# Optimization experiments

Measured on AMD Instinct MI355X. Metric: run time of the kernel, lower is better.

Reference implementation:

```python
import jax, jax.numpy as jnp
import numpy as np

N = 16384      # tokens
D_IN = 256     # input feature dim
D = 1024       # d_model
H = 2048       # expert hidden dim (2 * d_model)
E = 8          # n_experts
K = 2          # top_k
OUT = 2        # output classes
EPS = 1e-5


def layernorm(x, g, b):
    m = jnp.mean(x, axis=-1, keepdims=True)
    v = jnp.mean(jnp.square(x - m), axis=-1, keepdims=True)
    return (x - m) * jax.lax.rsqrt(v + EPS) * g + b


def setup_inputs() -> dict:
    key = jax.random.key(0)
    ks = jax.random.split(key, 10)
    s_in = 1.0 / np.sqrt(D_IN)
    s_d = 1.0 / np.sqrt(D)
    s_h = 1.0 / np.sqrt(H)
    return {
        "x": jax.random.normal(ks[0], (N, D_IN), jnp.float32),
        "w_in": jax.random.normal(ks[1], (D_IN, D), jnp.float32) * s_in,
        "b_in": jnp.zeros((D,), jnp.float32),
        "g_in": jnp.ones((D,), jnp.float32),
        "beta_in": jnp.zeros((D,), jnp.float32),
        "w_gate": jax.random.normal(ks[2], (D, E), jnp.float32) * s_d,
        "w1": jax.random.normal(ks[3], (E, D, H), jnp.float32) * s_d,
        "b1": jnp.zeros((E, H), jnp.float32),
        "w2": jax.random.normal(ks[4], (E, H, D), jnp.float32) * s_h,
        "b2": jnp.zeros((E, D), jnp.float32),
        "g_moe": jnp.ones((D,), jnp.float32),
        "beta_moe": jnp.zeros((D,), jnp.float32),
        "g_out": jnp.ones((D,), jnp.float32),
        "beta_out": jnp.zeros((D,), jnp.float32),
        "w_cls": jax.random.normal(ks[5], (D, OUT), jnp.float32) * s_d,
        "b_cls": jnp.zeros((OUT,), jnp.float32),
    }


def reference(x, w_in, b_in, g_in, beta_in, w_gate, w1, b1, w2, b2,
              g_moe, beta_moe, g_out, beta_out, w_cls, b_cls):
    # input projection + norm
    h = layernorm(x @ w_in + b_in, g_in, beta_in)            # [N, D]
    # router: softmax then top-k, renormalize over selected experts
    probs = jax.nn.softmax(h @ w_gate, axis=-1)              # [N, E]
    _, top_idx = jax.lax.top_k(probs, K)                     # [N, K]
    sel = jax.nn.one_hot(top_idx, E, dtype=probs.dtype).sum(axis=1)  # [N, E] 0/1
    gates = probs * sel
    gates = gates / (jnp.sum(gates, axis=-1, keepdims=True) + 1e-9)
    # experts: weighted combine; gate==0 tokens contribute nothing (same math
    # as the torch masked gather/scatter-add, dropout off in eval)
    mixed = jnp.zeros_like(h)
    for e in range(E):  # fixed, small expert count
        expert_out = jax.nn.gelu(h @ w1[e] + b1[e]) @ w2[e] + b2[e]  # [N, D]
        mixed = mixed + gates[:, e:e + 1] * expert_out
    out = layernorm(h + mixed, g_moe, beta_moe)
    out = layernorm(out, g_out, beta_out)
    return out @ w_cls + b_cls                               # [N, OUT]
```

## Files before the change

kernel.cpp:

```cpp
#include <hip/hip_runtime.h>
#include <hip/hip_bf16.h>

#define D_IN 256
#define DM   1024
#define HD   2048
#define NE   8
#define NTOK 16384

typedef __attribute__((ext_vector_type(8))) short short8;
typedef __attribute__((ext_vector_type(4))) float f32x4;
typedef unsigned int uint;

#define MT_TOFF1 0
#define MT_TOFF2 512
#define MT_CNT1  1536
#define MT_P1    1600
#define MT_OFF1  1664
#define MT_CNT2  1728
#define MT_PCNT2 1856
#define MT_TOTAL 1984

__device__ inline ushort f2bf(float v){
  __hip_bfloat16 b = __float2bfloat16(v);
  return *reinterpret_cast<ushort*>(&b);
}
__device__ inline float bf2f(ushort u){
  __hip_bfloat16 b = *reinterpret_cast<__hip_bfloat16*>(&u);
  return __bfloat162float(b);
}

__device__ inline float gelu_fast(float x){
  float u = 0.7978845608028654f * x * (1.0f + 0.044715f*x*x);
  return x / (1.0f + __expf(-2.0f*u));
}

__device__ inline void gload16(const void* g, void* l){
  __builtin_amdgcn_global_load_lds(
      (const __attribute__((address_space(1))) void*)g,
      (__attribute__((address_space(3))) void*)l, 16, 0, 0);
}

__global__ __launch_bounds__(256) void transpose_bf16_kernel(
    const float* __restrict__ src, ushort* __restrict__ dst, int R, int C)
{
  __shared__ float tile[32][33];
  int e = blockIdx.z;
  src += (size_t)e*R*C; dst += (size_t)e*R*C;
  int c0 = blockIdx.x*32, r0 = blockIdx.y*32;
  int tx = threadIdx.x & 31, ty = threadIdx.x >> 5;
  #pragma unroll
  for (int rr = ty; rr < 32; rr += 8)
    tile[rr][tx] = src[(size_t)(r0+rr)*C + c0+tx];
  __syncthreads();
  #pragma unroll
  for (int rr = ty; rr < 32; rr += 8)
    dst[(size_t)(c0+rr)*R + r0+tx] = f2bf(tile[tx][rr]);
}

__global__ __launch_bounds__(256) void split_x_kernel(
    const float* __restrict__ x, ushort* __restrict__ xs3)
{
  int g = blockIdx.x*256 + threadIdx.x;
  int e0 = g*4;
  int row = e0 >> 8, col = e0 & 255;
  f32x4 v = *(const f32x4*)(x + (size_t)row*D_IN + col);
  ushort4 hi, mi, lo;
  #pragma unroll
  for (int i=0;i<4;++i){
    float f = v[i];
    ushort h = f2bf(f);       float fh = bf2f(h);
    ushort m = f2bf(f - fh);  float fm = bf2f(m);
    ushort l = f2bf(f - fh - fm);
    ((ushort*)&hi)[i]=h; ((ushort*)&mi)[i]=m; ((ushort*)&lo)[i]=l;
  }
  ushort* base = xs3 + (size_t)row*768 + col;
  *(ushort4*)(base)       = hi;
  *(ushort4*)(base + 256) = mi;
  *(ushort4*)(base + 512) = lo;
}

__global__ __launch_bounds__(256) void transpose_split3_kernel(
    const float* __restrict__ src, ushort* __restrict__ dst)
{
  __shared__ float tile[32][33];
  int c0 = blockIdx.x*32, r0 = blockIdx.y*32;
  int tx = threadIdx.x & 31, ty = threadIdx.x >> 5;
  #pragma unroll
  for (int rr = ty; rr < 32; rr += 8)
    tile[rr][tx] = src[(size_t)(r0+rr)*DM + c0+tx];
  __syncthreads();
  #pragma unroll
  for (int rr = ty; rr < 32; rr += 8){
    float f = tile[tx][rr];
    ushort h = f2bf(f);       float fh = bf2f(h);
    ushort m = f2bf(f - fh);  float fm = bf2f(m);
    ushort l = f2bf(f - fh - fm);
    ushort* d = dst + (size_t)(c0+rr)*768 + r0 + tx;
    d[0]   = h;
    d[256] = m;
    d[512] = l;
  }
}

__global__ __launch_bounds__(256) void wgate_t_kernel(
    const float* __restrict__ w_gate, float* __restrict__ wgt)
{
  int e = blockIdx.x;
  for (int j = threadIdx.x; j < DM; j += 256)
    wgt[(size_t)e*DM + j] = w_gate[(size_t)j*NE + e];
}

__global__ __launch_bounds__(256) void gemm_router(
    const ushort* __restrict__ A,
    const ushort* __restrict__ BT,
    const float* __restrict__ b_in,
    float* __restrict__ y)
{
  __shared__ ushort As[128*32];
  __shared__ ushort Bs[128*32];
  const int tid = threadIdx.x;
  const int w = tid>>6, l = tid&63;
  const int wm = w>>1, wn = w&1;
  const int bm0 = blockIdx.y*128, bn0 = blockIdx.x*128;
  const int lr = l&15, lk = l>>4;
  const int rsub = l>>2, csub = (l&3)*8;

  const ushort* ag[2]; const ushort* bg[2];
  ushort* al[2]; ushort* bl[2];
  #pragma unroll
  for (int i=0;i<2;++i){
    int ra = bm0 + w*32 + i*16 + rsub;
    int rb = bn0 + w*32 + i*16 + rsub;
    ag[i] = A  + (size_t)ra*768 + csub;
    bg[i] = BT + (size_t)rb*768 + csub;
    al[i] = (ushort*)As + (w*32 + i*16)*32;
    bl[i] = (ushort*)Bs + (w*32 + i*16)*32;
  }

  f32x4 zero = {0.f,0.f,0.f,0.f};
  f32x4 acc[4][4];
  #pragma unroll
  for (int i=0;i<4;++i){
    #pragma unroll
    for (int j=0;j<4;++j) acc[i][j]=zero;
  }

  const int pq[6][2] = {{0,0},{256,0},{0,256},{256,256},{512,0},{0,512}};
  for (int t=0;t<6;++t){
    int pOff = pq[t][0], qOff = pq[t][1];
    for (int kt=0; kt<256; kt+=32){
      #pragma unroll
      for (int i=0;i<2;++i){
        gload16(ag[i]+pOff+kt, al[i]);
        gload16(bg[i]+qOff+kt, bl[i]);
      }
      __syncthreads();
      short8 af[4], bf[4];
      #pragma unroll
      for (int i=0;i<4;++i) af[i] = *(const short8*)(As + (wm*64 + i*16 + lr)*32 + lk*8);
      #pragma unroll
      for (int j=0;j<4;++j) bf[j] = *(const short8*)(Bs + (wn*64 + j*16 + lr)*32 + lk*8);
      #pragma unroll
      for (int i=0;i<4;++i){
        #pragma unroll
        for (int j=0;j<4;++j)
          acc[i][j] = __builtin_amdgcn_mfma_f32_16x16x32_bf16(af[i], bf[j], acc[i][j], 0, 0, 0);
      }
      __syncthreads();
    }
  }

  #pragma unroll
  for (int i=0;i<4;++i){
    #pragma unroll
    for (int j=0;j<4;++j){
      int n = bn0 + wn*64 + j*16 + lr;
      float bn_ = b_in[n];
      #pragma unroll
      for (int r=0;r<4;++r){
        int m = bm0 + wm*64 + i*16 + lk*4 + r;
        y[(size_t)m*DM + n] = acc[i][j][r] + bn_;
      }
    }
  }
}

__device__ inline double wredd(double v){
  #pragma unroll
  for (int o=32;o>0;o>>=1) v += __shfl_xor(v, o, 64);
  return v;
}

__global__ __launch_bounds__(256) void ln_router_kernel(
    const float* __restrict__ g_in, const float* __restrict__ beta_in,
    const float* __restrict__ wgt,
    ushort* __restrict__ hbf, float* __restrict__ resid,
    float* __restrict__ gates, int* __restrict__ selmask)
{
  int tok = blockIdx.x*4 + (threadIdx.x>>6);
  int l = threadIdx.x & 63;
  float* row = resid + (size_t)tok*DM;
  float u[16];
  double s=0.0, q=0.0;
  #pragma unroll
  for (int r=0;r<16;++r){ u[r]=row[l+64*r]; s+=u[r]; q+=(double)u[r]*u[r]; }
  s = wredd(s); q = wredd(q);
  double mean = s*(1.0/1024.0);
  double var  = q*(1.0/1024.0) - mean*mean;
  double rstd = 1.0/sqrt(var + 1e-5);

  double lg[NE];
  #pragma unroll
  for (int e=0;e<NE;++e) lg[e]=0.0;
  float hv[16];
  #pragma unroll
  for (int r=0;r<16;++r){
    int j = l + 64*r;
    double v = ((double)u[r]-mean)*rstd*(double)g_in[j] + (double)beta_in[j];
    hv[r] = (float)v;
    #pragma unroll
    for (int e=0;e<NE;++e) lg[e] += v*(double)wgt[(size_t)e*DM + j];
  }
  #pragma unroll
  for (int r=0;r<16;++r){
    int j = l + 64*r;
    row[j] = hv[r];
    hbf[(size_t)tok*DM + j] = f2bf(hv[r]);
  }
  #pragma unroll
  for (int e=0;e<NE;++e) lg[e] = wredd(lg[e]);

  if (l==0){
    double mx = lg[0];
    #pragma unroll
    for (int e=1;e<NE;++e) mx = lg[e]>mx ? lg[e] : mx;
    double p[NE]; double sum=0.0;
    #pragma unroll
    for (int e=0;e<NE;++e){ p[e]=exp(lg[e]-mx); sum+=p[e]; }
    #pragma unroll
    for (int e=0;e<NE;++e) p[e]/=sum;
    int i1=0;
    for (int e=1;e<NE;++e) if (p[e]>p[i1]) i1=e;
    int i2=-1;
    for (int e=0;e<NE;++e){ if (e==i1) continue; if (i2<0 || p[e]>p[i2]) i2=e; }
    double denom = p[i1]+p[i2]+1e-9;
    float g[NE];
    #pragma unroll
    for (int e=0;e<NE;++e) g[e]=0.f;
    g[i1]=(float)(p[i1]/denom);
    g[i2]=(float)(p[i2]/denom);
    #pragma unroll
    for (int e=0;e<NE;++e) gates[(size_t)tok*NE+e]=g[e];
    selmask[tok] = (1<<i1)|(1<<i2);
  }
}

__global__ __launch_bounds__(256) void builder_count(
    const int* __restrict__ selmask, uint* __restrict__ bc1, uint* __restrict__ bc2)
{
  __shared__ uint c1[8], c2s[16];
  int b = blockIdx.x, tid = threadIdx.x;
  if (tid<8) c1[tid]=0;
  if (tid<16) c2s[tid]=0;
  __syncthreads();
  int m = selmask[b*256+tid];
  int ea = __ffs(m)-1, eb = 31-__clz(m);
  atomicAdd(&c1[ea],1u); atomicAdd(&c1[eb],1u);
  atomicAdd(&c2s[ea],1u); atomicAdd(&c2s[8+eb],1u);
  __syncthreads();
  if (tid<8) bc1[b*8+tid]=c1[tid];
  if (tid<16) bc2[b*16+tid]=c2s[tid];
}

__global__ __launch_bounds__(256) void builder_scan(
    const uint* __restrict__ bc1, const uint* __restrict__ bc2,
    uint* __restrict__ meta, int nch, int TPC)
{
  int tid = threadIdx.x;
  int c = tid/24, k = tid%24;
  if (c < nch){
    if (k < 8){
      uint run=0;
      for (int b=c*TPC; b<(c+1)*TPC; ++b){ meta[MT_TOFF1 + b*8 + k] = run; run += bc1[b*8+k]; }
      meta[MT_CNT1 + c*8 + k] = run;
    } else {
      int k2 = k-8;
      uint run=0;
      for (int b=c*TPC; b<(c+1)*TPC; ++b){ meta[MT_TOFF2 + b*16 + k2] = run; run += bc2[b*16+k2]; }
      meta[MT_CNT2 + c*16 + k2] = run;
      meta[MT_PCNT2 + c*16 + k2] = ((run + 127u)/128u)*128u;
    }
  }
  __syncthreads();
  if (tid < nch){
    uint off=0;
    for (int e=0;e<8;++e){
      uint cn = meta[MT_CNT1 + tid*8 + e];
      uint p = ((cn+127u)/128u)*128u;
      meta[MT_P1 + tid*8 + e] = p;
      meta[MT_OFF1 + tid*8 + e] = off;
      off += p;
    }
  }
}

__device__ inline int exclscan256(int v, int* sc, int tid){
  sc[tid]=v; __syncthreads();
  #pragma unroll
  for (int o=1;o<256;o<<=1){
    int x = (tid>=o) ? sc[tid-o] : 0;
    __syncthreads();
    sc[tid]+=x;
    __syncthreads();
  }
  int incl = sc[tid]; __syncthreads();
  return incl - v;
}

__global__ __launch_bounds__(256) void builder_fill(
    const int* __restrict__ selmask, const uint* __restrict__ meta,
    int* __restrict__ ids1, int CH)
{
  __shared__ int sc[256];
  int b = blockIdx.x, tid = threadIdx.x;
  int t = b*256 + tid;
  int c = t / CH;
  int m = selmask[t];
  int ea = __ffs(m)-1, eb = 31-__clz(m);
  int ja=0, jb=0;
  for (int e=0;e<8;++e){
    int r0 = exclscan256((ea==e)?1:0, sc, tid);
    if (ea==e) ja = r0;
    int r1 = exclscan256((eb==e)?1:0, sc, tid);
    if (eb==e) jb = r1;
  }
  {
    uint j    = meta[MT_TOFF2 + b*16 + ea] + (uint)ja;
    ids1[(c*8+ea)*CH + j] = t;
  }
  {
    uint j    = meta[MT_TOFF2 + b*16 + 8 + eb] + (uint)jb;
    uint pos1 = meta[MT_CNT2 + c*16 + eb] + j;
    ids1[(c*8+eb)*CH + pos1] = t;
  }
}

__global__ __launch_bounds__(256) void gemm_ffn1(
    const ushort* __restrict__ Abase,
    const ushort* __restrict__ BT,
    const int*   __restrict__ rows,
    const uint*  __restrict__ pcnt,
    const uint*  __restrict__ off1,
    const float* __restrict__ bias,
    ushort* __restrict__ t1,
    int K, int N, int CH)
{
  const int e = blockIdx.z;
  const int bm0 = blockIdx.y*128;
  if ((uint)bm0 >= pcnt[e]) return;
  const int bn0 = blockIdx.x*128;

  __shared__ ushort As[128*32];
  __shared__ ushort Bs[128*32];
  const int tid = threadIdx.x;
  const int w = tid>>6, l = tid&63;
  const int wm = w>>1, wn = w&1;
  const int lr = l&15, lk = l>>4;
  const int rsub = l>>2, csub = (l&3)*8;

  const ushort* ag[2]; const ushort* bg[2];
  ushort* al[2]; ushort* bl[2];
  #pragma unroll
  for (int i=0;i<2;++i){
    int ra = w*32 + i*16 + rsub;
    int id = rows[e*CH + bm0 + ra];
    ag[i] = Abase + (size_t)id*K + csub;
    int rb = bn0 + w*32 + i*16 + rsub;
    bg[i] = BT + (size_t)e*N*K + (size_t)rb*K + csub;
    al[i] = (ushort*)As + (w*32 + i*16)*32;
    bl[i] = (ushort*)Bs + (w*32 + i*16)*32;
  }

  f32x4 zero = {0.f,0.f,0.f,0.f};
  f32x4 acc[4][4];
  #pragma unroll
  for (int i=0;i<4;++i){
    #pragma unroll
    for (int j=0;j<4;++j) acc[i][j]=zero;
  }

  for (int kt = 0; kt < K; kt += 32) {
    #pragma unroll
    for (int i=0;i<2;++i){
      gload16(ag[i]+kt, al[i]);
      gload16(bg[i]+kt, bl[i]);
    }
    __syncthreads();
    short8 af[4], bf[4];
    #pragma unroll
    for (int i=0;i<4;++i) af[i] = *(const short8*)(As + (wm*64 + i*16 + lr)*32 + lk*8);
    #pragma unroll
    for (int j=0;j<4;++j) bf[j] = *(const short8*)(Bs + (wn*64 + j*16 + lr)*32 + lk*8);
    #pragma unroll
    for (int i=0;i<4;++i){
      #pragma unroll
      for (int j=0;j<4;++j)
        acc[i][j] = __builtin_amdgcn_mfma_f32_16x16x32_bf16(af[i], bf[j], acc[i][j], 0, 0, 0);
    }
    __syncthreads();
  }

  #pragma unroll
  for (int i=0;i<4;++i){
    #pragma unroll
    for (int j=0;j<4;++j){
      int n = bn0 + wn*64 + j*16 + lr;
      float bn_ = bias[(size_t)e*N + n];
      #pragma unroll
      for (int r=0;r<4;++r){
        int mloc = wm*64 + i*16 + lk*4 + r;
        float v = acc[i][j][r] + bn_;
        size_t trow = (size_t)off1[e] + bm0 + mloc;
        t1[trow*N + n] = f2bf(gelu_fast(v));
      }
    }
  }
}

template<int SLOT>
__global__ __launch_bounds__(256) void gemm_ffn2(
    const ushort* __restrict__ t1,
    const ushort* __restrict__ BT,
    const int*   __restrict__ ids1,
    const uint*  __restrict__ cnt2,
    const uint*  __restrict__ pcnt2,
    const uint*  __restrict__ off1,
    const float* __restrict__ bias,
    const float* __restrict__ gates,
    float* __restrict__ resid,
    int K, int N, int CH)
{
  const int e = blockIdx.z;
  const int bm0 = blockIdx.y*128;
  if ((uint)bm0 >= pcnt2[SLOT*8 + e]) return;
  const uint scnt  = cnt2[SLOT*8 + e];
  const uint start = (SLOT==1) ? cnt2[e] : 0u;
  const int bn0 = blockIdx.x*128;

  __shared__ ushort As[128*32];
  __shared__ ushort Bs[128*32];
  const int tid = threadIdx.x;
  const int w = tid>>6, l = tid&63;
  const int wm = w>>1, wn = w&1;
  const int lr = l&15, lk = l>>4;
  const int rsub = l>>2, csub = (l&3)*8;

  const ushort* ag[2]; const ushort* bg[2];
  ushort* al[2]; ushort* bl[2];
  #pragma unroll
  for (int i=0;i<2;++i){
    int ra = w*32 + i*16 + rsub;
    size_t arow = (size_t)off1[e] + start + bm0 + ra;
    ag[i] = t1 + arow*K + csub;
    int rb = bn0 + w*32 + i*16 + rsub;
    bg[i] = BT + (size_t)e*N*K + (size_t)rb*K + csub;
    al[i] = (ushort*)As + (w*32 + i*16)*32;
    bl[i] = (ushort*)Bs + (w*32 + i*16)*32;
  }

  f32x4 zero = {0.f,0.f,0.f,0.f};
  f32x4 acc[4][4];
  #pragma unroll
  for (int i=0;i<4;++i){
    #pragma unroll
    for (int j=0;j<4;++j) acc[i][j]=zero;
  }

  for (int kt = 0; kt < K; kt += 32) {
    #pragma unroll
    for (int i=0;i<2;++i){
      gload16(ag[i]+kt, al[i]);
      gload16(bg[i]+kt, bl[i]);
    }
    __syncthreads();
    short8 af[4], bf[4];
    #pragma unroll
    for (int i=0;i<4;++i) af[i] = *(const short8*)(As + (wm*64 + i*16 + lr)*32 + lk*8);
    #pragma unroll
    for (int j=0;j<4;++j) bf[j] = *(const short8*)(Bs + (wn*64 + j*16 + lr)*32 + lk*8);
    #pragma unroll
    for (int i=0;i<4;++i){
      #pragma unroll
      for (int j=0;j<4;++j)
        acc[i][j] = __builtin_amdgcn_mfma_f32_16x16x32_bf16(af[i], bf[j], acc[i][j], 0, 0, 0);
    }
    __syncthreads();
  }

  #pragma unroll
  for (int i=0;i<4;++i){
    #pragma unroll
    for (int j=0;j<4;++j){
      int n = bn0 + wn*64 + j*16 + lr;
      float bn_ = bias[(size_t)e*N + n];
      #pragma unroll
      for (int r=0;r<4;++r){
        int mloc = wm*64 + i*16 + lk*4 + r;
        int mg = bm0 + mloc;
        if ((uint)mg < scnt){
          int tok = ids1[e*CH + (int)start + mg];
          float g = gates[(size_t)tok*NE + e];
          resid[(size_t)tok*N + n] += g*(acc[i][j][r] + bn_);
        }
      }
    }
  }
}

__global__ __launch_bounds__(256) void final_kernel(
    const float* __restrict__ resid,
    const float* __restrict__ g_moe, const float* __restrict__ beta_moe,
    const float* __restrict__ g_out, const float* __restrict__ beta_out,
    const float* __restrict__ w_cls, const float* __restrict__ b_cls,
    float* __restrict__ out)
{
  int tok = blockIdx.x*4 + (threadIdx.x>>6);
  int l = threadIdx.x & 63;
  const float* row = resid + (size_t)tok*DM;
  float u[16];
  double s=0.0,q=0.0;
  #pragma unroll
  for (int r=0;r<16;++r){ u[r]=row[l + 64*r]; s+=u[r]; q+=(double)u[r]*u[r]; }
  s=wredd(s); q=wredd(q);
  double m1 = s*(1.0/1024.0), v1 = q*(1.0/1024.0)-m1*m1;
  double rs1 = 1.0/sqrt(v1+1e-5);
  float tv[16]; double s2=0.0,q2=0.0;
  #pragma unroll
  for (int r=0;r<16;++r){
    int j = l+64*r;
    float vv = (float)((u[r]-m1)*rs1)*g_moe[j] + beta_moe[j];
    tv[r]=vv; s2+=vv; q2+=(double)vv*vv;
  }
  s2=wredd(s2); q2=wredd(q2);
  double m2=s2*(1.0/1024.0), v2=q2*(1.0/1024.0)-m2*m2;
  double rs2=1.0/sqrt(v2+1e-5);
  double p0=0.0,p1=0.0;
  #pragma unroll
  for (int r=0;r<16;++r){
    int j=l+64*r;
    double y=((double)tv[r]-m2)*rs2*(double)g_out[j]+(double)beta_out[j];
    p0+=y*(double)w_cls[j*2]; p1+=y*(double)w_cls[j*2+1];
  }
  p0=wredd(p0); p1=wredd(p1);
  if (l==0){
    out[(size_t)tok*2  ]=(float)(p0+(double)b_cls[0]);
    out[(size_t)tok*2+1]=(float)(p1+(double)b_cls[1]);
  }
}

extern "C" void kernel_launch(void* const* d_in, const int* in_sizes, int n_in,
                              void* d_out, int out_size, void* d_ws, size_t ws_size,
                              hipStream_t stream)
{
  (void)in_sizes; (void)n_in; (void)out_size;
  const float* x       = (const float*)d_in[0];
  const float* w_in    = (const float*)d_in[1];
  const float* b_in    = (const float*)d_in[2];
  const float* g_in    = (const float*)d_in[3];
  const float* beta_in = (const float*)d_in[4];
  const float* w_gate  = (const float*)d_in[5];
  const float* w1      = (const float*)d_in[6];
  const float* b1      = (const float*)d_in[7];
  const float* w2      = (const float*)d_in[8];
  const float* b2      = (const float*)d_in[9];
  const float* g_moe   = (const float*)d_in[10];
  const float* beta_mo = (const float*)d_in[11];
  const float* g_out   = (const float*)d_in[12];
  const float* beta_ou = (const float*)d_in[13];
  const float* w_cls   = (const float*)d_in[14];
  const float* b_cls   = (const float*)d_in[15];
  float* out = (float*)d_out;

  char* p = (char*)d_ws;
  ushort* w1t   = (ushort*)p; p += (size_t)NE*HD*DM*2;
  ushort* w2t   = (ushort*)p; p += (size_t)NE*DM*HD*2;
  ushort* hbf   = (ushort*)p; p += (size_t)NTOK*DM*2;
  float*  resid = (float*)p;  p += (size_t)NTOK*DM*4;
  float*  gates = (float*)p;  p += (size_t)NTOK*NE*4;
  int*    selmk = (int*)p;    p += (size_t)NTOK*4;
  int*    ids1  = (int*)p;    p += (size_t)NE*NTOK*4;
  ushort* wt3   = (ushort*)p; p += (size_t)DM*768*2;
  float*  wgt   = (float*)p;  p += (size_t)NE*DM*4;
  uint*   bc1   = (uint*)p;   p += (size_t)64*8*4;
  uint*   bc2   = (uint*)p;   p += (size_t)64*16*4;
  uint*   meta  = (uint*)p;   p += (size_t)MT_TOTAL*4;
  size_t fixed = (size_t)(p - (char*)d_ws);

  const size_t xs3_bytes = (size_t)NTOK*768*2;
  size_t t1b1 = ((size_t)2*NTOK        + 2048)*HD*2;
  size_t t1b2 = ((size_t)2*(NTOK/2)    + 2048)*HD*2;
  size_t t1b4 = ((size_t)2*(NTOK/4)    + 2048)*HD*2;
  int nch = 8;
  if      (ws_size >= fixed + (t1b1 > xs3_bytes ? t1b1 : xs3_bytes)) nch = 1;
  else if (ws_size >= fixed + (t1b2 > xs3_bytes ? t1b2 : xs3_bytes)) nch = 2;
  else if (ws_size >= fixed + (t1b4 > xs3_bytes ? t1b4 : xs3_bytes)) nch = 4;
  const int CH  = NTOK/nch;
  const int TPC = CH/256;
  ushort* t1  = (ushort*)p;
  ushort* xs3 = (ushort*)p;

  split_x_kernel<<<dim3(NTOK*D_IN/4/256), 256, 0, stream>>>(x, xs3);
  transpose_split3_kernel<<<dim3(DM/32, D_IN/32), 256, 0, stream>>>(w_in, wt3);
  wgate_t_kernel<<<dim3(NE), 256, 0, stream>>>(w_gate, wgt);
  transpose_bf16_kernel<<<dim3(HD/32, DM/32, NE), 256, 0, stream>>>(w1, w1t, DM, HD);
  transpose_bf16_kernel<<<dim3(DM/32, HD/32, NE), 256, 0, stream>>>(w2, w2t, HD, DM);

  gemm_router<<<dim3(DM/128, NTOK/128), 256, 0, stream>>>(xs3, wt3, b_in, resid);
  ln_router_kernel<<<dim3(NTOK/4), 256, 0, stream>>>(g_in, beta_in, wgt,
                                                     hbf, resid, gates, selmk);

  hipMemsetAsync(ids1, 0, (size_t)NE*NTOK*4, stream);

  builder_count<<<dim3(NTOK/256), 256, 0, stream>>>(selmk, bc1, bc2);
  builder_scan<<<dim3(1), 256, 0, stream>>>(bc1, bc2, meta, nch, TPC);
  builder_fill<<<dim3(NTOK/256), 256, 0, stream>>>(selmk, meta, ids1, CH);

  for (int c = 0; c < nch; ++c) {
    gemm_ffn1<<<dim3(HD/128, CH/128, NE), 256, 0, stream>>>(
        hbf, w1t, ids1 + (size_t)c*8*CH,
        meta+MT_P1+c*8, meta+MT_OFF1+c*8, b1, t1, DM, HD, CH);
    gemm_ffn2<0><<<dim3(DM/128, CH/128, NE), 256, 0, stream>>>(
        t1, w2t, ids1 + (size_t)c*8*CH,
        meta+MT_CNT2+c*16, meta+MT_PCNT2+c*16, meta+MT_OFF1+c*8,
        b2, gates, resid, HD, DM, CH);
    gemm_ffn2<1><<<dim3(DM/128, CH/128, NE), 256, 0, stream>>>(
        t1, w2t, ids1 + (size_t)c*8*CH,
        meta+MT_CNT2+c*16, meta+MT_PCNT2+c*16, meta+MT_OFF1+c*8,
        b2, gates, resid, HD, DM, CH);
  }

  final_kernel<<<dim3(NTOK/4), 256, 0, stream>>>(resid, g_moe, beta_mo, g_out, beta_ou,
                                                 w_cls, b_cls, out);
}
```

Baseline: 984.5 us.

## Double-buffer LDS tiles in router and expert GEMMs to overlap loads with MFMA

```diff
diff --git a/kernel.cpp b/kernel.cpp
--- a/kernel.cpp
+++ b/kernel.cpp
@@ -116,8 +116,8 @@
     const float* __restrict__ b_in,
     float* __restrict__ y)
 {
-  __shared__ ushort As[128*32];
-  __shared__ ushort Bs[128*32];
+  __shared__ ushort As[2][128*32];
+  __shared__ ushort Bs[2][128*32];
   const int tid = threadIdx.x;
   const int w = tid>>6, l = tid&63;
   const int wm = w>>1, wn = w&1;
@@ -126,48 +126,48 @@
   const int rsub = l>>2, csub = (l&3)*8;
 
   const ushort* ag[2]; const ushort* bg[2];
-  ushort* al[2]; ushort* bl[2];
+  int aslot[2];
   #pragma unroll
   for (int i=0;i<2;++i){
     int ra = bm0 + w*32 + i*16 + rsub;
     int rb = bn0 + w*32 + i*16 + rsub;
     ag[i] = A  + (size_t)ra*768 + csub;
     bg[i] = BT + (size_t)rb*768 + csub;
-    al[i] = (ushort*)As + (w*32 + i*16)*32;
-    bl[i] = (ushort*)Bs + (w*32 + i*16)*32;
-  }
-
-  f32x4 zero = {0.f,0.f,0.f,0.f};
-  f32x4 acc[4][4];
-  #pragma unroll
-  for (int i=0;i<4;++i){
-    #pragma unroll
-    for (int j=0;j<4;++j) acc[i][j]=zero;
-  }
-
-  const int pq[6][2] = {{0,0},{256,0},{0,256},{256,256},{512,0},{0,512}};
-  for (int t=0;t<6;++t){
-    int pOff = pq[t][0], qOff = pq[t][1];
-    for (int kt=0; kt<256; kt+=32){
+    aslot[i] = (w*32 + i*16)*32;
+  }
+
+  const int pOffT[6] = {0,256,0,256,512,0};
+  const int qOffT[6] = {0,0,256,256,0,512};
+  auto stage = [&](int db, int t){
+    int pOff = pOffT[t>>3] + (t&7)*32;
+    int qOff = qOffT[t>>3] + (t&7)*32;
+    #pragma unroll
+    for (int i=0;i<2;++i){
+      gload16(ag[i]+pOff, (ushort*)As[db] + aslot[i]);
+      gload16(bg[i]+qOff, (ushort*)Bs[db] + aslot[i]);
+    }
+  };
+
+  f32x4 acc[4][4] = {};
+  const int NK = 48;
+  stage(0, 0);
+  for (int t=0; t<NK; ++t){
+    const int cur = t&1;
+    if (t+1 < NK){ stage(cur^1, t+1); asm volatile("s_waitcnt vmcnt(4)" ::: "memory"); }
+    else         {                    asm volatile("s_waitcnt vmcnt(0)" ::: "memory"); }
+    __builtin_amdgcn_s_barrier();
+    short8 af[4], bf[4];
+    #pragma unroll
+    for (int i=0;i<4;++i) af[i] = *(const short8*)(As[cur] + (wm*64 + i*16 + lr)*32 + lk*8);
+    #pragma unroll
+    for (int j=0;j<4;++j) bf[j] = *(const short8*)(Bs[cur] + (wn*64 + j*16 + lr)*32 + lk*8);
+    #pragma unroll
+    for (int i=0;i<4;++i){
       #pragma unroll
-      for (int i=0;i<2;++i){
-        gload16(ag[i]+pOff+kt, al[i]);
-        gload16(bg[i]+qOff+kt, bl[i]);
-      }
-      __syncthreads();
-      short8 af[4], bf[4];
-      #pragma unroll
-      for (int i=0;i<4;++i) af[i] = *(const short8*)(As + (wm*64 + i*16 + lr)*32 + lk*8);
-      #pragma unroll
-      for (int j=0;j<4;++j) bf[j] = *(const short8*)(Bs + (wn*64 + j*16 + lr)*32 + lk*8);
-      #pragma unroll
-      for (int i=0;i<4;++i){
-        #pragma unroll
-        for (int j=0;j<4;++j)
-          acc[i][j] = __builtin_amdgcn_mfma_f32_16x16x32_bf16(af[i], bf[j], acc[i][j], 0, 0, 0);
-      }
-      __syncthreads();
-    }
+      for (int j=0;j<4;++j)
+        acc[i][j] = __builtin_amdgcn_mfma_f32_16x16x32_bf16(af[i], bf[j], acc[i][j], 0, 0, 0);
+    }
+    __builtin_amdgcn_s_barrier();
   }
 
   #pragma unroll
@@ -360,8 +360,8 @@
   if ((uint)bm0 >= pcnt[e]) return;
   const int bn0 = blockIdx.x*128;
 
-  __shared__ ushort As[128*32];
-  __shared__ ushort Bs[128*32];
+  __shared__ ushort As[2][128*32];
+  __shared__ ushort Bs[2][128*32];
   const int tid = threadIdx.x;
   const int w = tid>>6, l = tid&63;
   const int wm = w>>1, wn = w&1;
@@ -369,7 +369,7 @@
   const int rsub = l>>2, csub = (l&3)*8;
 
   const ushort* ag[2]; const ushort* bg[2];
-  ushort* al[2]; ushort* bl[2];
+  int slot[2];
   #pragma unroll
   for (int i=0;i<2;++i){
     int ra = w*32 + i*16 + rsub;
@@ -377,37 +377,37 @@
     ag[i] = Abase + (size_t)id*K + csub;
     int rb = bn0 + w*32 + i*16 + rsub;
     bg[i] = BT + (size_t)e*N*K + (size_t)rb*K + csub;
-    al[i] = (ushort*)As + (w*32 + i*16)*32;
-    bl[i] = (ushort*)Bs + (w*32 + i*16)*32;
-  }
-
-  f32x4 zero = {0.f,0.f,0.f,0.f};
-  f32x4 acc[4][4];
-  #pragma unroll
-  for (int i=0;i<4;++i){
-    #pragma unroll
-    for (int j=0;j<4;++j) acc[i][j]=zero;
-  }
-
-  for (int kt = 0; kt < K; kt += 32) {
+    slot[i] = (w*32 + i*16)*32;
+  }
+
+  auto stage = [&](int db, int kt){
     #pragma unroll
     for (int i=0;i<2;++i){
-      gload16(ag[i]+kt, al[i]);
-      gload16(bg[i]+kt, bl[i]);
-    }
-    __syncthreads();
+      gload16(ag[i]+kt, (ushort*)As[db] + slot[i]);
+      gload16(bg[i]+kt, (ushort*)Bs[db] + slot[i]);
+    }
+  };
+
+  f32x4 acc[4][4] = {};
+  const int NK = K>>5;
+  stage(0, 0);
+  for (int t=0; t<NK; ++t){
+    const int cur = t&1;
+    if (t+1 < NK){ stage(cur^1, (t+1)<<5); asm volatile("s_waitcnt vmcnt(4)" ::: "memory"); }
+    else         {                          asm volatile("s_waitcnt vmcnt(0)" ::: "memory"); }
+    __builtin_amdgcn_s_barrier();
     short8 af[4], bf[4];
     #pragma unroll
-    for (int i=0;i<4;++i) af[i] = *(const short8*)(As + (wm*64 + i*16 + lr)*32 + lk*8);
-    #pragma unroll
-    for (int j=0;j<4;++j) bf[j] = *(const short8*)(Bs + (wn*64 + j*16 + lr)*32 + lk*8);
+    for (int i=0;i<4;++i) af[i] = *(const short8*)(As[cur] + (wm*64 + i*16 + lr)*32 + lk*8);
+    #pragma unroll
+    for (int j=0;j<4;++j) bf[j] = *(const short8*)(Bs[cur] + (wn*64 + j*16 + lr)*32 + lk*8);
     #pragma unroll
     for (int i=0;i<4;++i){
       #pragma unroll
       for (int j=0;j<4;++j)
         acc[i][j] = __builtin_amdgcn_mfma_f32_16x16x32_bf16(af[i], bf[j], acc[i][j], 0, 0, 0);
     }
-    __syncthreads();
+    __builtin_amdgcn_s_barrier();
   }
 
   #pragma unroll
@@ -447,8 +447,8 @@
   const uint start = (SLOT==1) ? cnt2[e] : 0u;
   const int bn0 = blockIdx.x*128;
 
-  __shared__ ushort As[128*32];
-  __shared__ ushort Bs[128*32];
+  __shared__ ushort As[2][128*32];
+  __shared__ ushort Bs[2][128*32];
   const int tid = threadIdx.x;
   const int w = tid>>6, l = tid&63;
   const int wm = w>>1, wn = w&1;
@@ -456,7 +456,7 @@
   const int rsub = l>>2, csub = (l&3)*8;
 
   const ushort* ag[2]; const ushort* bg[2];
-  ushort* al[2]; ushort* bl[2];
+  int slot[2];
   #pragma unroll
   for (int i=0;i<2;++i){
     int ra = w*32 + i*16 + rsub;
@@ -464,37 +464,37 @@
     ag[i] = t1 + arow*K + csub;
     int rb = bn0 + w*32 + i*16 + rsub;
     bg[i] = BT + (size_t)e*N*K + (size_t)rb*K + csub;
-    al[i] = (ushort*)As + (w*32 + i*16)*32;
-    bl[i] = (ushort*)Bs + (w*32 + i*16)*32;
-  }
-
-  f32x4 zero = {0.f,0.f,0.f,0.f};
-  f32x4 acc[4][4];
-  #pragma unroll
-  for (int i=0;i<4;++i){
-    #pragma unroll
-    for (int j=0;j<4;++j) acc[i][j]=zero;
-  }
-
-  for (int kt = 0; kt < K; kt += 32) {
+    slot[i] = (w*32 + i*16)*32;
+  }
+
+  auto stage = [&](int db, int kt){
     #pragma unroll
     for (int i=0;i<2;++i){
-      gload16(ag[i]+kt, al[i]);
-      gload16(bg[i]+kt, bl[i]);
-    }
-    __syncthreads();
+      gload16(ag[i]+kt, (ushort*)As[db] + slot[i]);
+      gload16(bg[i]+kt, (ushort*)Bs[db] + slot[i]);
+    }
+  };
+
+  f32x4 acc[4][4] = {};
+  const int NK = K>>5;
+  stage(0, 0);
+  for (int t=0; t<NK; ++t){
+    const int cur = t&1;
+    if (t+1 < NK){ stage(cur^1, (t+1)<<5); asm volatile("s_waitcnt vmcnt(4)" ::: "memory"); }
+    else         {                          asm volatile("s_waitcnt vmcnt(0)" ::: "memory"); }
+    __builtin_amdgcn_s_barrier();
     short8 af[4], bf[4];
     #pragma unroll
-    for (int i=0;i<4;++i) af[i] = *(const short8*)(As + (wm*64 + i*16 + lr)*32 + lk*8);
-    #pragma unroll
-    for (int j=0;j<4;++j) bf[j] = *(const short8*)(Bs + (wn*64 + j*16 + lr)*32 + lk*8);
+    for (int i=0;i<4;++i) af[i] = *(const short8*)(As[cur] + (wm*64 + i*16 + lr)*32 + lk*8);
+    #pragma unroll
+    for (int j=0;j<4;++j) bf[j] = *(const short8*)(Bs[cur] + (wn*64 + j*16 + lr)*32 + lk*8);
     #pragma unroll
     for (int i=0;i<4;++i){
       #pragma unroll
       for (int j=0;j<4;++j)
         acc[i][j] = __builtin_amdgcn_mfma_f32_16x16x32_bf16(af[i], bf[j], acc[i][j], 0, 0, 0);
     }
-    __syncthreads();
+    __builtin_amdgcn_s_barrier();
   }
 
   #pragma unroll
```

Measured after the change: 891.2 us. 9.5% less time.
